# Kernel tuning notes

Measured on AMD Instinct MI355X. Metric: run time of the kernel, lower is better.

Reference implementation:

```python
import jax, jax.numpy as jnp
import numpy as np

B, T, D_IN, H, N_LAYERS, D_OUT = 256, 512, 128, 512, 3, 1


def setup_inputs() -> dict:
    key = jax.random.key(0)
    ks = jax.random.split(key, 20)
    s = 1.0 / np.sqrt(H)
    inp = {"x": jax.random.normal(ks[0], (B, T, D_IN), dtype=jnp.float32)}
    k = 1
    for l in range(N_LAYERS):
        d_in = D_IN if l == 0 else H
        inp[f"W_ih_{l}"] = jax.random.uniform(ks[k], (4 * H, d_in), minval=-s, maxval=s); k += 1
        inp[f"W_hh_{l}"] = jax.random.uniform(ks[k], (4 * H, H), minval=-s, maxval=s); k += 1
        inp[f"b_ih_{l}"] = jax.random.uniform(ks[k], (4 * H,), minval=-s, maxval=s); k += 1
        inp[f"b_hh_{l}"] = jax.random.uniform(ks[k], (4 * H,), minval=-s, maxval=s); k += 1
    inp["W_fc"] = jax.random.uniform(ks[k], (D_OUT, H), minval=-s, maxval=s); k += 1
    inp["b_fc"] = jax.random.uniform(ks[k], (D_OUT,), minval=-s, maxval=s)
    return inp


def _lstm_layer(x, W_ih, W_hh, b_ih, b_hh):
    # x: [B, T, d_in] -> hs: [B, T, H]. PyTorch gate order: i, f, g, o.
    xg = jnp.einsum("btd,gd->btg", x, W_ih) + b_ih + b_hh  # precompute input proj [B,T,4H]
    Hh = W_hh.shape[1]
    Bb = x.shape[0]

    def step(carry, xg_t):
        h, c = carry
        g = xg_t + h @ W_hh.T  # [B, 4H]
        i, f, gg, o = jnp.split(g, 4, axis=-1)
        c = jax.nn.sigmoid(f) * c + jax.nn.sigmoid(i) * jnp.tanh(gg)
        h = jax.nn.sigmoid(o) * jnp.tanh(c)
        return (h, c), h

    h0 = jnp.zeros((Bb, Hh), x.dtype)
    (_, _), hs = jax.lax.scan(step, (h0, h0), jnp.swapaxes(xg, 0, 1))
    return jnp.swapaxes(hs, 0, 1)


def reference(x, W_ih_0, W_hh_0, b_ih_0, b_hh_0,
              W_ih_1, W_hh_1, b_ih_1, b_hh_1,
              W_ih_2, W_hh_2, b_ih_2, b_hh_2,
              W_fc, b_fc):
    # Eval mode: inter-layer dropout (p=0.4) is identity.
    h = _lstm_layer(x, W_ih_0, W_hh_0, b_ih_0, b_hh_0)
    h = _lstm_layer(h, W_ih_1, W_hh_1, b_ih_1, b_hh_1)
    h = _lstm_layer(h, W_ih_2, W_hh_2, b_ih_2, b_hh_2)
    return h[:, -1, :] @ W_fc.T + b_fc  # [B, D_OUT]
```

## Files before the change

kernel.cpp:

```cpp
#include <hip/hip_runtime.h>

#define B_   256
#define T_   512
#define DIN_ 128
#define H_   512
#define G4_  2048

typedef __bf16 bf16_t;
typedef __bf16 bf16x8 __attribute__((ext_vector_type(8)));
typedef __bf16 bf16x4 __attribute__((ext_vector_type(4)));
typedef float  f32x4  __attribute__((ext_vector_type(4)));
typedef float  f32x16 __attribute__((ext_vector_type(16)));

__device__ __forceinline__ void gload16cc(const void* g, void* l) {
  __builtin_amdgcn_global_load_lds(
      (const __attribute__((address_space(1))) unsigned int*)g,
      (__attribute__((address_space(3))) unsigned int*)l, 16, 0, 17);
}
__device__ __forceinline__ int fload(const int* p) {
  return __hip_atomic_load(p, __ATOMIC_RELAXED, __HIP_MEMORY_SCOPE_AGENT);
}

__global__ void cast_f32_bf16(const float* __restrict__ s, bf16_t* __restrict__ d, int n) {
  int i = (blockIdx.x * 256 + threadIdx.x) * 4;
  if (i >= n) return;
  float4 v = *(const float4*)(s + i);
  bf16x4 o;
  o[0] = (bf16_t)v.x; o[1] = (bf16_t)v.y; o[2] = (bf16_t)v.z; o[3] = (bf16_t)v.w;
  *(bf16x4*)(d + i) = o;
}

__global__ void cast_strided(const float* __restrict__ s, bf16_t* __restrict__ d,
                             int Ks, int Kd, int coff) {
  int npr = Ks >> 3;
  int i = blockIdx.x * 256 + threadIdx.x;
  if (i >= 2048 * npr) return;
  int row = i / npr, j = i - row * npr;
  const float* sp = s + (size_t)row * Ks + j * 8;
  float4 v0 = *(const float4*)sp;
  float4 v1 = *(const float4*)(sp + 4);
  bf16x8 o;
  o[0] = (bf16_t)v0.x; o[1] = (bf16_t)v0.y; o[2] = (bf16_t)v0.z; o[3] = (bf16_t)v0.w;
  o[4] = (bf16_t)v1.x; o[5] = (bf16_t)v1.y; o[6] = (bf16_t)v1.z; o[7] = (bf16_t)v1.w;
  *(bf16x8*)(d + (size_t)row * Kd + coff + j * 8) = o;
}

__global__ void bias_sum(const float* __restrict__ a, const float* __restrict__ b,
                         float* __restrict__ o, int n) {
  int i = blockIdx.x * 256 + threadIdx.x;
  if (i < n) o[i] = a[i] + b[i];
}

#define RING_N (8 * 256 * 512)
#define XG_N   (8 * 256 * 2048)
#define FSTR   16

__device__ __forceinline__ void l0_loop(
    char* smem, const bf16_t* __restrict__ xbf, const bf16_t* __restrict__ wcl,
    const float* __restrict__ bias_l, bf16_t* ringOwn, int* flags, int* xgf,
    int bg, int ug)
{
  constexpr int ROWB = 1280;
  const int tid  = threadIdx.x;
  const int lane = tid & 63;
  const int wv   = tid >> 6;
  const int g    = wv & 3;
  const int kh   = wv >> 2;
  const int r32  = lane & 31;
  const int l5   = lane >> 5;
  const int u0   = ug * 32;
  const int t0x  = kh * 4;
  const int t0h  = 8 + kh * 16;

  bf16x8 wfrag[20];
  {
    const bf16_t* wrow = wcl + (size_t)(g * 512 + u0 + r32) * 640 + l5 * 8;
    #pragma unroll
    for (int i = 0; i < 4; ++i)  wfrag[i]     = *(const bf16x8*)(wrow + (t0x + i) * 16);
    #pragma unroll
    for (int i = 0; i < 16; ++i) wfrag[4 + i] = *(const bf16x8*)(wrow + (t0h + i) * 16);
  }
  const int um = tid >> 3;
  const int uq = tid & 7;
  float bsv[4][4];
  #pragma unroll
  for (int g2 = 0; g2 < 4; ++g2)
    #pragma unroll
    for (int q = 0; q < 4; ++q)
      bsv[g2][q] = bias_l[g2 * 512 + u0 + uq * 4 + q];

  float cst[4] = {0.f, 0.f, 0.f, 0.f};
  float* gp = (float*)smem;

  int* fl_own = flags + (0 * 4 + bg) * FSTR;
  int* bpf    = xgf + (0 * 4 + bg) * FSTR;

  for (int s = 0; s < 512; ++s) {
    const int slot  = s & 7;
    const int slot2 = (s - 1) & 7;
    {
      int r0 = tid >> 4, c0 = tid & 15;
      bf16x8 v0 = *(const bf16x8*)(xbf + ((size_t)(bg * 64 + r0) * T_ + s) * 128 + c0 * 8);
      int i1 = 512 + tid, r1 = i1 >> 4, c1 = i1 & 15;
      bf16x8 v1 = *(const bf16x8*)(xbf + ((size_t)(bg * 64 + r1) * T_ + s) * 128 + c1 * 8);
      *(bf16x8*)(smem + r0 * ROWB + (c0 ^ (r0 & 15)) * 16) = v0;
      *(bf16x8*)(smem + r1 * ROWB + (c1 ^ (r1 & 15)) * 16) = v1;
    }
    __syncthreads();
    f32x16 acc0 = {}, acc1 = {};
    #pragma unroll
    for (int i = 0; i < 2; ++i) {
      const int px = ((t0x + i) * 2 + l5) ^ (r32 & 15);
      bf16x8 a0 = *(const bf16x8*)(smem + r32 * ROWB + px * 16);
      bf16x8 a1 = *(const bf16x8*)(smem + (32 + r32) * ROWB + px * 16);
      acc0 = __builtin_amdgcn_mfma_f32_32x32x16_bf16(a0, wfrag[i], acc0, 0, 0, 0);
      acc1 = __builtin_amdgcn_mfma_f32_32x32x16_bf16(a1, wfrag[i], acc1, 0, 0, 0);
    }
    if (tid == 0) {
      if (s > 0)
        while (fload(fl_own + (s - 1) * 4 * FSTR) < 16) __builtin_amdgcn_s_sleep(1);
      if (s >= 8)
        while (fload(bpf + (s - 8) * 4 * FSTR) < 8) __builtin_amdgcn_s_sleep(1);
    }
    __syncthreads();
    {
      const bf16_t* ownS = ringOwn + (size_t)slot2 * (256 * 512) + (size_t)(bg * 64) * 512;
      #pragma unroll
      for (int i = 0; i < 8; ++i) {
        int r = i * 8 + wv;
        gload16cc(ownS + r * 512 + (lane ^ (r & 15)) * 8, smem + r * ROWB + 256);
      }
    }
    #pragma unroll
    for (int i = 2; i < 4; ++i) {
      const int px = ((t0x + i) * 2 + l5) ^ (r32 & 15);
      bf16x8 a0 = *(const bf16x8*)(smem + r32 * ROWB + px * 16);
      bf16x8 a1 = *(const bf16x8*)(smem + (32 + r32) * ROWB + px * 16);
      acc0 = __builtin_amdgcn_mfma_f32_32x32x16_bf16(a0, wfrag[i], acc0, 0, 0, 0);
      acc1 = __builtin_amdgcn_mfma_f32_32x32x16_bf16(a1, wfrag[i], acc1, 0, 0, 0);
    }
    __syncthreads();
    #pragma unroll
    for (int i = 0; i < 16; ++i) {
      const int px = ((t0h + i) * 2 + l5) ^ (r32 & 15);
      bf16x8 a0 = *(const bf16x8*)(smem + r32 * ROWB + px * 16);
      bf16x8 a1 = *(const bf16x8*)(smem + (32 + r32) * ROWB + px * 16);
      acc0 = __builtin_amdgcn_mfma_f32_32x32x16_bf16(a0, wfrag[4 + i], acc0, 0, 0, 0);
      acc1 = __builtin_amdgcn_mfma_f32_32x32x16_bf16(a1, wfrag[4 + i], acc1, 0, 0, 0);
    }
    __syncthreads();
    {
      const int base = kh * 8192 + g * 32 + r32;
      #pragma unroll
      for (int reg = 0; reg < 16; ++reg) {
        int mr = (reg & 3) + 8 * (reg >> 2) + 4 * l5;
        gp[base + mr * 128]        = acc0[reg];
        gp[base + (32 + mr) * 128] = acc1[reg];
      }
    }
    __syncthreads();
    union { bf16x4 v; unsigned long long u; } pk;
    {
      f32x4 gv[4];
      #pragma unroll
      for (int g2 = 0; g2 < 4; ++g2) {
        f32x4 p0 = *(const f32x4*)&gp[um * 128 + g2 * 32 + uq * 4];
        f32x4 p1 = *(const f32x4*)&gp[8192 + um * 128 + g2 * 32 + uq * 4];
        #pragma unroll
        for (int q = 0; q < 4; ++q) gv[g2][q] = p0[q] + p1[q];
      }
      #pragma unroll
      for (int q = 0; q < 4; ++q) {
        float i_ = gv[0][q] + bsv[0][q];
        float f_ = gv[1][q] + bsv[1][q];
        float g_ = gv[2][q] + bsv[2][q];
        float o_ = gv[3][q] + bsv[3][q];
        float si = 1.f / (1.f + __expf(-i_));
        float sf = 1.f / (1.f + __expf(-f_));
        float so = 1.f / (1.f + __expf(-o_));
        float tg = 2.f / (1.f + __expf(-2.f * g_)) - 1.f;
        float cv = sf * cst[q] + si * tg;
        cst[q] = cv;
        float th = 2.f / (1.f + __expf(-2.f * cv)) - 1.f;
        pk.v[q] = (bf16_t)(so * th);
      }
    }
    {
      int b = bg * 64 + um;
      bf16_t* dst = ringOwn + (size_t)slot * (256 * 512) + (size_t)b * 512 + u0 + uq * 4;
      (void)__hip_atomic_exchange((unsigned long long*)dst, pk.u,
                                  __ATOMIC_RELAXED, __HIP_MEMORY_SCOPE_AGENT);
    }
    __syncthreads();
    if (tid == 0) atomicAdd(fl_own + s * 4 * FSTR, 1);
  }
}

__device__ __forceinline__ void main_loop(
    char* smem, const bf16_t* __restrict__ wcl, const float* __restrict__ bias_l,
    const float* __restrict__ xgRing, bf16_t* ringOwn, float* __restrict__ hsf,
    int* flags, int* xgf, int layer, int bg, int ug)
{
  const int tid  = threadIdx.x;
  const int lane = tid & 63;
  const int wv   = tid >> 6;
  const int g    = wv & 3;
  const int kh   = wv >> 2;
  const int r32  = lane & 31;
  const int l5   = lane >> 5;
  const int u0   = ug * 32;

  bf16x8 wfrag[16];
  {
    const bf16_t* wrow = wcl + (size_t)(g * 512 + u0 + r32) * 1024 + 512 + kh * 256 + l5 * 8;
    #pragma unroll
    for (int i = 0; i < 16; ++i) wfrag[i] = *(const bf16x8*)(wrow + i * 16);
  }
  const int um = tid >> 3;
  const int uq = tid & 7;
  float bsv[4][4];
  #pragma unroll
  for (int g2 = 0; g2 < 4; ++g2)
    #pragma unroll
    for (int q = 0; q < 4; ++q)
      bsv[g2][q] = bias_l[g2 * 512 + u0 + uq * 4 + q];

  float cst[4] = {0.f, 0.f, 0.f, 0.f};

  int* fl_own = flags + ((layer * 512) * 4 + bg) * FSTR;
  int* xgf_in = xgf + (((layer - 1) * 512) * 4 + bg) * FSTR;
  int* xgf_bp = xgf + ((1 * 512) * 4 + bg) * FSTR;

  for (int s = 0; s < 512; ++s) {
    const int slot  = s & 7;
    const int slot2 = (s - 1) & 7;
    if (tid == 0) {
      while (fload(xgf_in + s * 4 * FSTR) < 8) __builtin_amdgcn_s_sleep(1);
      if (s > 0)
        while (fload(fl_own + (s - 1) * 4 * FSTR) < 16) __builtin_amdgcn_s_sleep(1);
      if (layer == 1 && s >= 8)
        while (fload(xgf_bp + (s - 8) * 4 * FSTR) < 8) __builtin_amdgcn_s_sleep(1);
    }
    __syncthreads();
    {
      const bf16_t* ownS = ringOwn + (size_t)slot2 * (256 * 512) + (size_t)(bg * 64) * 512;
      #pragma unroll
      for (int i = 0; i < 8; ++i) {
        int r = i * 8 + wv;
        gload16cc(ownS + r * 512 + (lane ^ (r & 15)) * 8, smem + r * 1024);
      }
      const float* xgS = xgRing + (size_t)slot * (256 * 2048) + (size_t)(bg * 64) * 2048;
      #pragma unroll
      for (int i = 0; i < 4; ++i) {
        int id = (i * 8 + wv) * 64 + lane;
        int row = id >> 5, sub = id & 31, g2 = sub >> 3, cp = sub & 7;
        gload16cc(xgS + (size_t)row * 2048 + g2 * 512 + u0 + cp * 4,
                  smem + 65536 + (i * 8 + wv) * 1024);
      }
    }
    __syncthreads();
    f32x16 acc0 = {}, acc1 = {};
    #pragma unroll
    for (int i = 0; i < 16; ++i) {
      const int c  = (kh * 16 + i) * 2 + l5;
      const int px = c ^ (r32 & 15);
      bf16x8 a0 = *(const bf16x8*)(smem + r32 * 1024 + px * 16);
      bf16x8 a1 = *(const bf16x8*)(smem + (32 + r32) * 1024 + px * 16);
      acc0 = __builtin_amdgcn_mfma_f32_32x32x16_bf16(a0, wfrag[i], acc0, 0, 0, 0);
      acc1 = __builtin_amdgcn_mfma_f32_32x32x16_bf16(a1, wfrag[i], acc1, 0, 0, 0);
    }
    __syncthreads();
    {
      char* pb = smem + kh * 32768 + (g * 32 + r32) * 4;
      #pragma unroll
      for (int reg = 0; reg < 16; ++reg) {
        int mr = (reg & 3) + 8 * (reg >> 2) + 4 * l5;
        *(float*)(pb + mr * 512)        = acc0[reg];
        *(float*)(pb + (32 + mr) * 512) = acc1[reg];
      }
    }
    __syncthreads();
    union { bf16x4 v; unsigned long long u; } pk;
    f32x4 hvf;
    {
      const char* gpb = smem + um * 512;
      const char* xgb = smem + 65536 + um * 512;
      f32x4 gvv[4];
      #pragma unroll
      for (int g2 = 0; g2 < 4; ++g2) {
        f32x4 p0 = *(const f32x4*)(gpb + (g2 * 32 + uq * 4) * 4);
        f32x4 p1 = *(const f32x4*)(gpb + 32768 + (g2 * 32 + uq * 4) * 4);
        f32x4 xv = *(const f32x4*)(xgb + g2 * 128 + uq * 16);
        #pragma unroll
        for (int q = 0; q < 4; ++q) gvv[g2][q] = p0[q] + p1[q] + xv[q];
      }
      #pragma unroll
      for (int q = 0; q < 4; ++q) {
        float i_ = gvv[0][q] + bsv[0][q];
        float f_ = gvv[1][q] + bsv[1][q];
        float g_ = gvv[2][q] + bsv[2][q];
        float o_ = gvv[3][q] + bsv[3][q];
        float si = 1.f / (1.f + __expf(-i_));
        float sf = 1.f / (1.f + __expf(-f_));
        float so = 1.f / (1.f + __expf(-o_));
        float tg = 2.f / (1.f + __expf(-2.f * g_)) - 1.f;
        float cv = sf * cst[q] + si * tg;
        cst[q] = cv;
        float th = 2.f / (1.f + __expf(-2.f * cv)) - 1.f;
        hvf[q] = so * th;
        pk.v[q] = (bf16_t)hvf[q];
      }
    }
    {
      int b = bg * 64 + um;
      bf16_t* dst = ringOwn + (size_t)slot * (256 * 512) + (size_t)b * 512 + u0 + uq * 4;
      (void)__hip_atomic_exchange((unsigned long long*)dst, pk.u,
                                  __ATOMIC_RELAXED, __HIP_MEMORY_SCOPE_AGENT);
      if (layer == 2 && s == 511)
        *(f32x4*)(hsf + (size_t)b * 512 + u0 + uq * 4) = hvf;
    }
    __syncthreads();
    if (tid == 0) atomicAdd(fl_own + s * 4 * FSTR, 1);
  }
}

__device__ __forceinline__ void helper_loop(
    char* smem, const bf16_t* __restrict__ wihl, const bf16_t* __restrict__ ringPrev,
    float* __restrict__ xgRing, int* flags, int* xgf, int hl, int bg, int ng)
{
  const int tid  = threadIdx.x;
  const int lane = tid & 63;
  const int wv   = tid >> 6;
  const int r32  = lane & 31;
  const int l5   = lane >> 5;
  const int n0   = ng * 256 + wv * 32;

  bf16x8 wfrag[32];
  {
    const bf16_t* wrow = wihl + (size_t)(n0 + r32) * 1024 + l5 * 8;
    #pragma unroll
    for (int i = 0; i < 32; ++i) wfrag[i] = *(const bf16x8*)(wrow + i * 16);
  }
  int* fl_prev = flags + (((hl - 1) * 512) * 4 + bg) * FSTR;
  int* fl_cons = flags + ((hl * 512) * 4 + bg) * FSTR;
  int* xgf_own = xgf + (((hl - 1) * 512) * 4 + bg) * FSTR;

  for (int s = 0; s < 512; ++s) {
    const int slot = s & 7;
    if (tid == 0) {
      while (fload(fl_prev + s * 4 * FSTR) < 16) __builtin_amdgcn_s_sleep(1);
      if (s >= 8)
        while (fload(fl_cons + (s - 8) * 4 * FSTR) < 16) __builtin_amdgcn_s_sleep(1);
    }
    __syncthreads();
    {
      const bf16_t* src = ringPrev + (size_t)slot * (256 * 512) + (size_t)(bg * 64) * 512;
      #pragma unroll
      for (int i = 0; i < 8; ++i) {
        int r = i * 8 + wv;
        gload16cc(src + r * 512 + (lane ^ (r & 15)) * 8, smem + r * 1024);
      }
    }
    __syncthreads();
    f32x16 acc0 = {}, acc1 = {};
    #pragma unroll
    for (int i = 0; i < 32; ++i) {
      const int px = (i * 2 + l5) ^ (r32 & 15);
      bf16x8 a0 = *(const bf16x8*)(smem + r32 * 1024 + px * 16);
      bf16x8 a1 = *(const bf16x8*)(smem + (32 + r32) * 1024 + px * 16);
      acc0 = __builtin_amdgcn_mfma_f32_32x32x16_bf16(a0, wfrag[i], acc0, 0, 0, 0);
      acc1 = __builtin_amdgcn_mfma_f32_32x32x16_bf16(a1, wfrag[i], acc1, 0, 0, 0);
    }
    {
      float* dst = xgRing + (size_t)slot * (256 * 2048) + (size_t)(bg * 64) * 2048 + n0 + r32;
      #pragma unroll
      for (int reg = 0; reg < 16; ++reg) {
        int mr = (reg & 3) + 8 * (reg >> 2) + 4 * l5;
        __hip_atomic_store(dst + (size_t)mr * 2048, acc0[reg],
                           __ATOMIC_RELAXED, __HIP_MEMORY_SCOPE_AGENT);
        __hip_atomic_store(dst + (size_t)(32 + mr) * 2048, acc1[reg],
                           __ATOMIC_RELAXED, __HIP_MEMORY_SCOPE_AGENT);
      }
    }
    __syncthreads();
    if (tid == 0) atomicAdd(xgf_own + s * 4 * FSTR, 1);
  }
}

__global__ __launch_bounds__(512, 2)
void lstm_persist(const bf16_t* __restrict__ xbf, const bf16_t* __restrict__ wc,
                  const float* __restrict__ bias, bf16_t* __restrict__ rings,
                  float* __restrict__ xg, float* __restrict__ hsf,
                  int* __restrict__ flags)
{
  __shared__ __align__(16) char smem[131072];
  int* xgf = flags + 3 * 512 * 4 * FSTR;
  const int bid = blockIdx.x;
  if (bid < 192) {
    const int layer = bid >> 6;
    const int bg    = (bid >> 4) & 3;
    const int ug    = bid & 15;
    bf16_t* ringOwn = rings + (size_t)layer * RING_N;
    if (layer == 0) {
      l0_loop(smem, xbf, wc, bias, ringOwn, flags, xgf, bg, ug);
    } else {
      const bf16_t* wcl = wc + 2048 * 640 + (size_t)(layer - 1) * 2048 * 1024;
      const float* xgR  = xg + (size_t)(layer - 1) * XG_N;
      main_loop(smem, wcl, bias + layer * 2048, xgR, ringOwn, hsf, flags, xgf,
                layer, bg, ug);
    }
  } else {
    const int hid = bid - 192;
    const int hl  = 1 + (hid >> 5);
    const int bg  = (hid >> 3) & 3;
    const int ng  = hid & 7;
    const bf16_t* wihl = wc + 2048 * 640 + (size_t)(hl - 1) * 2048 * 1024;
    const bf16_t* ringPrev = rings + (size_t)(hl - 1) * RING_N;
    float* xgR = xg + (size_t)(hl - 1) * XG_N;
    helper_loop(smem, wihl, ringPrev, xgR, flags, xgf, hl, bg, ng);
  }
}

__global__ void fc_kernel(const float* __restrict__ h, const float* __restrict__ Wfc,
                          const float* __restrict__ bfc, float* __restrict__ out) {
  int b = blockIdx.x;
  int l = threadIdx.x;
  const float* hp = h + (size_t)b * H_;
  float acc = 0.f;
  #pragma unroll
  for (int i = 0; i < 8; ++i) acc += hp[l + i * 64] * Wfc[l + i * 64];
  #pragma unroll
  for (int off = 32; off; off >>= 1) acc += __shfl_down(acc, off, 64);
  if (l == 0) out[b] = acc + bfc[0];
}

extern "C" void kernel_launch(void* const* d_in, const int* in_sizes, int n_in,
                              void* d_out, int out_size, void* d_ws, size_t ws_size,
                              hipStream_t stream) {
  const float* x        = (const float*)d_in[0];
  const float* Wih_f[3] = {(const float*)d_in[1], (const float*)d_in[5], (const float*)d_in[9]};
  const float* Whh_f[3] = {(const float*)d_in[2], (const float*)d_in[6], (const float*)d_in[10]};
  const float* bih_f[3] = {(const float*)d_in[3], (const float*)d_in[7], (const float*)d_in[11]};
  const float* bhh_f[3] = {(const float*)d_in[4], (const float*)d_in[8], (const float*)d_in[12]};
  const float* Wfc = (const float*)d_in[13];
  const float* bfc = (const float*)d_in[14];

  const size_t FLAGS_BYTES = (size_t)(3 * 512 * 4 + 2 * 512 * 4) * FSTR * 4;

  char* ws = (char*)d_ws;
  size_t off = 0;
  auto take = [&](size_t bytes) { char* p = ws + off; off = (off + bytes + 255) & ~255ULL; return p; };
  bf16_t* XBF   = (bf16_t*)take((size_t)B_ * T_ * DIN_ * 2);
  bf16_t* WC    = (bf16_t*)take((size_t)(2048*640 + 2*2048*1024) * 2);
  float*  BIAS  = (float*) take(3 * 2048 * 4);
  bf16_t* RINGS = (bf16_t*)take((size_t)3 * RING_N * 2);
  float*  XG    = (float*) take((size_t)2 * XG_N * 4);
  float*  HSF   = (float*) take((size_t)B_ * H_ * 4);
  int*    FLAGS = (int*)   take(FLAGS_BYTES);

  bf16_t* WC1 = WC + 2048 * 640;
  bf16_t* WC2 = WC1 + 2048 * 1024;

  cast_f32_bf16<<<16384, 256, 0, stream>>>(x, XBF, B_ * T_ * DIN_);
  cast_strided<<<128, 256, 0, stream>>>(Wih_f[0], WC,  128, 640, 0);
  cast_strided<<<512, 256, 0, stream>>>(Whh_f[0], WC,  512, 640, 128);
  cast_strided<<<512, 256, 0, stream>>>(Wih_f[1], WC1, 512, 1024, 0);
  cast_strided<<<512, 256, 0, stream>>>(Whh_f[1], WC1, 512, 1024, 512);
  cast_strided<<<512, 256, 0, stream>>>(Wih_f[2], WC2, 512, 1024, 0);
  cast_strided<<<512, 256, 0, stream>>>(Whh_f[2], WC2, 512, 1024, 512);
  for (int l = 0; l < 3; ++l)
    bias_sum<<<8, 256, 0, stream>>>(bih_f[l], bhh_f[l], BIAS + l * 2048, G4_);
  hipMemsetAsync(RINGS, 0, (size_t)3 * RING_N * 2, stream);
  hipMemsetAsync(FLAGS, 0, FLAGS_BYTES, stream);

  lstm_persist<<<256, 512, 0, stream>>>(XBF, WC, BIAS, RINGS, XG, HSF, FLAGS);
  fc_kernel<<<B_, 64, 0, stream>>>(HSF, Wfc, bfc, (float*)d_out);
}
```

Baseline: 3.311 ms.

## Offload layer-0 input projection to helper blocks via a 16-slot xg ring

Layer-0 recurrent blocks previously computed the x·W_ih projection inline on every step, which lengthens the serial critical path. Helper blocks now compute that projection 8 steps ahead, using their spare upper waves, and write it into a new 16-slot fp32 ring guarded by a new flag array. Layer 0 then runs the same templated main_loop as the other layers and only reads the precomputed gates. The cost is extra helper work, fp32 ring traffic and extra flag synchronisation.

```diff
diff --git a/kernel.cpp b/kernel.cpp
--- a/kernel.cpp
+++ b/kernel.cpp
@@ -51,16 +51,21 @@
   if (i < n) o[i] = a[i] + b[i];
 }
 
-#define RING_N (8 * 256 * 512)
-#define XG_N   (8 * 256 * 2048)
-#define FSTR   16
-
-__device__ __forceinline__ void l0_loop(
-    char* smem, const bf16_t* __restrict__ xbf, const bf16_t* __restrict__ wcl,
-    const float* __restrict__ bias_l, bf16_t* ringOwn, int* flags, int* xgf,
-    int bg, int ug)
+#define RING_N  (8 * 256 * 512)
+#define XG_N    (8 * 256 * 2048)
+#define XG0_N   (16 * 256 * 2048)
+#define FSTR    16
+
+template<int LAYER>
+__device__ __forceinline__ void main_loop(
+    char* smem, const bf16_t* __restrict__ wcl, const float* __restrict__ bias_l,
+    const float* __restrict__ xgRing, bf16_t* ringOwn, float* __restrict__ hsf,
+    int* flags, int* xgf, int* xgf0, int bg, int ug)
 {
-  constexpr int ROWB = 1280;
+  constexpr int KLW   = LAYER ? 1024 : 640;
+  constexpr int WOFF  = LAYER ? 512 : 128;
+  constexpr int XMASK = LAYER ? 7 : 15;
+  constexpr int XTH   = LAYER ? 8 : 16;
   const int tid  = threadIdx.x;
   const int lane = tid & 63;
   const int wv   = tid >> 6;
@@ -69,16 +74,12 @@
   const int r32  = lane & 31;
   const int l5   = lane >> 5;
   const int u0   = ug * 32;
-  const int t0x  = kh * 4;
-  const int t0h  = 8 + kh * 16;
-
-  bf16x8 wfrag[20];
+
+  bf16x8 wfrag[16];
   {
-    const bf16_t* wrow = wcl + (size_t)(g * 512 + u0 + r32) * 640 + l5 * 8;
+    const bf16_t* wrow = wcl + (size_t)(g * 512 + u0 + r32) * KLW + WOFF + kh * 256 + l5 * 8;
     #pragma unroll
-    for (int i = 0; i < 4; ++i)  wfrag[i]     = *(const bf16x8*)(wrow + (t0x + i) * 16);
-    #pragma unroll
-    for (int i = 0; i < 16; ++i) wfrag[4 + i] = *(const bf16x8*)(wrow + (t0h + i) * 16);
+    for (int i = 0; i < 16; ++i) wfrag[i] = *(const bf16x8*)(wrow + i * 16);
   }
   const int um = tid >> 3;
   const int uq = tid & 7;
@@ -90,156 +91,24 @@
       bsv[g2][q] = bias_l[g2 * 512 + u0 + uq * 4 + q];
 
   float cst[4] = {0.f, 0.f, 0.f, 0.f};
-  float* gp = (float*)smem;
-
-  int* fl_own = flags + (0 * 4 + bg) * FSTR;
-  int* bpf    = xgf + (0 * 4 + bg) * FSTR;
+
+  int* fl_own = flags + ((LAYER * 512) * 4 + bg) * FSTR;
+  int* xin    = (LAYER == 0) ? (xgf0 + bg * FSTR)
+                             : (xgf + (((LAYER - 1) * 512) * 4 + bg) * FSTR);
+  int* bp     = (LAYER == 0) ? (xgf + (0 * 4 + bg) * FSTR)
+              : (LAYER == 1) ? (xgf + ((1 * 512) * 4 + bg) * FSTR)
+              : (int*)nullptr;
 
   for (int s = 0; s < 512; ++s) {
     const int slot  = s & 7;
     const int slot2 = (s - 1) & 7;
-    {
-      int r0 = tid >> 4, c0 = tid & 15;
-      bf16x8 v0 = *(const bf16x8*)(xbf + ((size_t)(bg * 64 + r0) * T_ + s) * 128 + c0 * 8);
-      int i1 = 512 + tid, r1 = i1 >> 4, c1 = i1 & 15;
-      bf16x8 v1 = *(const bf16x8*)(xbf + ((size_t)(bg * 64 + r1) * T_ + s) * 128 + c1 * 8);
-      *(bf16x8*)(smem + r0 * ROWB + (c0 ^ (r0 & 15)) * 16) = v0;
-      *(bf16x8*)(smem + r1 * ROWB + (c1 ^ (r1 & 15)) * 16) = v1;
-    }
-    __syncthreads();
-    f32x16 acc0 = {}, acc1 = {};
-    #pragma unroll
-    for (int i = 0; i < 2; ++i) {
-      const int px = ((t0x + i) * 2 + l5) ^ (r32 & 15);
-      bf16x8 a0 = *(const bf16x8*)(smem + r32 * ROWB + px * 16);
-      bf16x8 a1 = *(const bf16x8*)(smem + (32 + r32) * ROWB + px * 16);
-      acc0 = __builtin_amdgcn_mfma_f32_32x32x16_bf16(a0, wfrag[i], acc0, 0, 0, 0);
-      acc1 = __builtin_amdgcn_mfma_f32_32x32x16_bf16(a1, wfrag[i], acc1, 0, 0, 0);
-    }
+    const int xslot = s & XMASK;
     if (tid == 0) {
+      while (fload(xin + s * 4 * FSTR) < XTH) __builtin_amdgcn_s_sleep(1);
       if (s > 0)
         while (fload(fl_own + (s - 1) * 4 * FSTR) < 16) __builtin_amdgcn_s_sleep(1);
-      if (s >= 8)
-        while (fload(bpf + (s - 8) * 4 * FSTR) < 8) __builtin_amdgcn_s_sleep(1);
-    }
-    __syncthreads();
-    {
-      const bf16_t* ownS = ringOwn + (size_t)slot2 * (256 * 512) + (size_t)(bg * 64) * 512;
-      #pragma unroll
-      for (int i = 0; i < 8; ++i) {
-        int r = i * 8 + wv;
-        gload16cc(ownS + r * 512 + (lane ^ (r & 15)) * 8, smem + r * ROWB + 256);
-      }
-    }
-    #pragma unroll
-    for (int i = 2; i < 4; ++i) {
-      const int px = ((t0x + i) * 2 + l5) ^ (r32 & 15);
-      bf16x8 a0 = *(const bf16x8*)(smem + r32 * ROWB + px * 16);
-      bf16x8 a1 = *(const bf16x8*)(smem + (32 + r32) * ROWB + px * 16);
-      acc0 = __builtin_amdgcn_mfma_f32_32x32x16_bf16(a0, wfrag[i], acc0, 0, 0, 0);
-      acc1 = __builtin_amdgcn_mfma_f32_32x32x16_bf16(a1, wfrag[i], acc1, 0, 0, 0);
-    }
-    __syncthreads();
-    #pragma unroll
-    for (int i = 0; i < 16; ++i) {
-      const int px = ((t0h + i) * 2 + l5) ^ (r32 & 15);
-      bf16x8 a0 = *(const bf16x8*)(smem + r32 * ROWB + px * 16);
-      bf16x8 a1 = *(const bf16x8*)(smem + (32 + r32) * ROWB + px * 16);
-      acc0 = __builtin_amdgcn_mfma_f32_32x32x16_bf16(a0, wfrag[4 + i], acc0, 0, 0, 0);
-      acc1 = __builtin_amdgcn_mfma_f32_32x32x16_bf16(a1, wfrag[4 + i], acc1, 0, 0, 0);
-    }
-    __syncthreads();
-    {
-      const int base = kh * 8192 + g * 32 + r32;
-      #pragma unroll
-      for (int reg = 0; reg < 16; ++reg) {
-        int mr = (reg & 3) + 8 * (reg >> 2) + 4 * l5;
-        gp[base + mr * 128]        = acc0[reg];
-        gp[base + (32 + mr) * 128] = acc1[reg];
-      }
-    }
-    __syncthreads();
-    union { bf16x4 v; unsigned long long u; } pk;
-    {
-      f32x4 gv[4];
-      #pragma unroll
-      for (int g2 = 0; g2 < 4; ++g2) {
-        f32x4 p0 = *(const f32x4*)&gp[um * 128 + g2 * 32 + uq * 4];
-        f32x4 p1 = *(const f32x4*)&gp[8192 + um * 128 + g2 * 32 + uq * 4];
-        #pragma unroll
-        for (int q = 0; q < 4; ++q) gv[g2][q] = p0[q] + p1[q];
-      }
-      #pragma unroll
-      for (int q = 0; q < 4; ++q) {
-        float i_ = gv[0][q] + bsv[0][q];
-        float f_ = gv[1][q] + bsv[1][q];
-        float g_ = gv[2][q] + bsv[2][q];
-        float o_ = gv[3][q] + bsv[3][q];
-        float si = 1.f / (1.f + __expf(-i_));
-        float sf = 1.f / (1.f + __expf(-f_));
-        float so = 1.f / (1.f + __expf(-o_));
-        float tg = 2.f / (1.f + __expf(-2.f * g_)) - 1.f;
-        float cv = sf * cst[q] + si * tg;
-        cst[q] = cv;
-        float th = 2.f / (1.f + __expf(-2.f * cv)) - 1.f;
-        pk.v[q] = (bf16_t)(so * th);
-      }
-    }
-    {
-      int b = bg * 64 + um;
-      bf16_t* dst = ringOwn + (size_t)slot * (256 * 512) + (size_t)b * 512 + u0 + uq * 4;
-      (void)__hip_atomic_exchange((unsigned long long*)dst, pk.u,
-                                  __ATOMIC_RELAXED, __HIP_MEMORY_SCOPE_AGENT);
-    }
-    __syncthreads();
-    if (tid == 0) atomicAdd(fl_own + s * 4 * FSTR, 1);
-  }
-}
-
-__device__ __forceinline__ void main_loop(
-    char* smem, const bf16_t* __restrict__ wcl, const float* __restrict__ bias_l,
-    const float* __restrict__ xgRing, bf16_t* ringOwn, float* __restrict__ hsf,
-    int* flags, int* xgf, int layer, int bg, int ug)
-{
-  const int tid  = threadIdx.x;
-  const int lane = tid & 63;
-  const int wv   = tid >> 6;
-  const int g    = wv & 3;
-  const int kh   = wv >> 2;
-  const int r32  = lane & 31;
-  const int l5   = lane >> 5;
-  const int u0   = ug * 32;
-
-  bf16x8 wfrag[16];
-  {
-    const bf16_t* wrow = wcl + (size_t)(g * 512 + u0 + r32) * 1024 + 512 + kh * 256 + l5 * 8;
-    #pragma unroll
-    for (int i = 0; i < 16; ++i) wfrag[i] = *(const bf16x8*)(wrow + i * 16);
-  }
-  const int um = tid >> 3;
-  const int uq = tid & 7;
-  float bsv[4][4];
-  #pragma unroll
-  for (int g2 = 0; g2 < 4; ++g2)
-    #pragma unroll
-    for (int q = 0; q < 4; ++q)
-      bsv[g2][q] = bias_l[g2 * 512 + u0 + uq * 4 + q];
-
-  float cst[4] = {0.f, 0.f, 0.f, 0.f};
-
-  int* fl_own = flags + ((layer * 512) * 4 + bg) * FSTR;
-  int* xgf_in = xgf + (((layer - 1) * 512) * 4 + bg) * FSTR;
-  int* xgf_bp = xgf + ((1 * 512) * 4 + bg) * FSTR;
-
-  for (int s = 0; s < 512; ++s) {
-    const int slot  = s & 7;
-    const int slot2 = (s - 1) & 7;
-    if (tid == 0) {
-      while (fload(xgf_in + s * 4 * FSTR) < 8) __builtin_amdgcn_s_sleep(1);
-      if (s > 0)
-        while (fload(fl_own + (s - 1) * 4 * FSTR) < 16) __builtin_amdgcn_s_sleep(1);
-      if (layer == 1 && s >= 8)
-        while (fload(xgf_bp + (s - 8) * 4 * FSTR) < 8) __builtin_amdgcn_s_sleep(1);
+      if (LAYER < 2 && s >= 8)
+        while (fload(bp + (s - 8) * 4 * FSTR) < 8) __builtin_amdgcn_s_sleep(1);
     }
     __syncthreads();
     {
@@ -249,7 +118,7 @@
         int r = i * 8 + wv;
         gload16cc(ownS + r * 512 + (lane ^ (r & 15)) * 8, smem + r * 1024);
       }
-      const float* xgS = xgRing + (size_t)slot * (256 * 2048) + (size_t)(bg * 64) * 2048;
+      const float* xgS = xgRing + (size_t)xslot * (256 * 2048) + (size_t)(bg * 64) * 2048;
       #pragma unroll
       for (int i = 0; i < 4; ++i) {
         int id = (i * 8 + wv) * 64 + lane;
@@ -316,7 +185,7 @@
       bf16_t* dst = ringOwn + (size_t)slot * (256 * 512) + (size_t)b * 512 + u0 + uq * 4;
       (void)__hip_atomic_exchange((unsigned long long*)dst, pk.u,
                                   __ATOMIC_RELAXED, __HIP_MEMORY_SCOPE_AGENT);
-      if (layer == 2 && s == 511)
+      if (LAYER == 2 && s == 511)
         *(f32x4*)(hsf + (size_t)b * 512 + u0 + uq * 4) = hvf;
     }
     __syncthreads();
@@ -324,9 +193,12 @@
   }
 }
 
+template<int HL>
 __device__ __forceinline__ void helper_loop(
-    char* smem, const bf16_t* __restrict__ wihl, const bf16_t* __restrict__ ringPrev,
-    float* __restrict__ xgRing, int* flags, int* xgf, int hl, int bg, int ng)
+    char* smem, const bf16_t* __restrict__ wihl, const bf16_t* __restrict__ wc0,
+    const bf16_t* __restrict__ xbf, const bf16_t* __restrict__ ringPrev,
+    float* __restrict__ xgRing, float* __restrict__ xg0Ring,
+    int* flags, int* xgf, int* xgf0, int bg, int ng)
 {
   const int tid  = threadIdx.x;
   const int lane = tid & 63;
@@ -334,6 +206,7 @@
   const int r32  = lane & 31;
   const int l5   = lane >> 5;
   const int n0   = ng * 256 + wv * 32;
+  const int cs   = (HL - 1) * 8 + ng;
 
   bf16x8 wfrag[32];
   {
@@ -341,19 +214,22 @@
     #pragma unroll
     for (int i = 0; i < 32; ++i) wfrag[i] = *(const bf16x8*)(wrow + i * 16);
   }
-  int* fl_prev = flags + (((hl - 1) * 512) * 4 + bg) * FSTR;
-  int* fl_cons = flags + ((hl * 512) * 4 + bg) * FSTR;
-  int* xgf_own = xgf + (((hl - 1) * 512) * 4 + bg) * FSTR;
-
-  for (int s = 0; s < 512; ++s) {
-    const int slot = s & 7;
-    if (tid == 0) {
+  int* fl_prev  = flags + (((HL - 1) * 512) * 4 + bg) * FSTR;
+  int* fl_cons  = flags + ((HL * 512) * 4 + bg) * FSTR;
+  int* xgf_own  = xgf + (((HL - 1) * 512) * 4 + bg) * FSTR;
+  int* xgf0_own = xgf0 + bg * FSTR;
+
+  for (int s = -8; s < 512; ++s) {
+    const bool doH = (s >= 0);
+    const bool doX = (s + 8 < 512);
+    const int  slot = s & 7;
+    if (doH && tid == 0) {
       while (fload(fl_prev + s * 4 * FSTR) < 16) __builtin_amdgcn_s_sleep(1);
       if (s >= 8)
         while (fload(fl_cons + (s - 8) * 4 * FSTR) < 16) __builtin_amdgcn_s_sleep(1);
     }
     __syncthreads();
-    {
+    if (doH) {
       const bf16_t* src = ringPrev + (size_t)slot * (256 * 512) + (size_t)(bg * 64) * 512;
       #pragma unroll
       for (int i = 0; i < 8; ++i) {
@@ -361,17 +237,25 @@
         gload16cc(src + r * 512 + (lane ^ (r & 15)) * 8, smem + r * 1024);
       }
     }
-    __syncthreads();
-    f32x16 acc0 = {}, acc1 = {};
-    #pragma unroll
-    for (int i = 0; i < 32; ++i) {
-      const int px = (i * 2 + l5) ^ (r32 & 15);
-      bf16x8 a0 = *(const bf16x8*)(smem + r32 * 1024 + px * 16);
-      bf16x8 a1 = *(const bf16x8*)(smem + (32 + r32) * 1024 + px * 16);
-      acc0 = __builtin_amdgcn_mfma_f32_32x32x16_bf16(a0, wfrag[i], acc0, 0, 0, 0);
-      acc1 = __builtin_amdgcn_mfma_f32_32x32x16_bf16(a1, wfrag[i], acc1, 0, 0, 0);
-    }
-    {
+    if (doX) {
+      #pragma unroll
+      for (int i2 = 0; i2 < 2; ++i2) {
+        int id = i2 * 512 + tid, r = id >> 4, cx = id & 15;
+        bf16x8 v = *(const bf16x8*)(xbf + ((size_t)(bg * 64 + r) * T_ + (s + 8)) * 128 + cx * 8);
+        *(bf16x8*)(smem + 65536 + r * 256 + (cx ^ (r & 15)) * 16) = v;
+      }
+    }
+    __syncthreads();
+    if (doH) {
+      f32x16 acc0 = {}, acc1 = {};
+      #pragma unroll
+      for (int i = 0; i < 32; ++i) {
+        const int px = (i * 2 + l5) ^ (r32 & 15);
+        bf16x8 a0 = *(const bf16x8*)(smem + r32 * 1024 + px * 16);
+        bf16x8 a1 = *(const bf16x8*)(smem + (32 + r32) * 1024 + px * 16);
+        acc0 = __builtin_amdgcn_mfma_f32_32x32x16_bf16(a0, wfrag[i], acc0, 0, 0, 0);
+        acc1 = __builtin_amdgcn_mfma_f32_32x32x16_bf16(a1, wfrag[i], acc1, 0, 0, 0);
+      }
       float* dst = xgRing + (size_t)slot * (256 * 2048) + (size_t)(bg * 64) * 2048 + n0 + r32;
       #pragma unroll
       for (int reg = 0; reg < 16; ++reg) {
@@ -382,42 +266,74 @@
                            __ATOMIC_RELAXED, __HIP_MEMORY_SCOPE_AGENT);
       }
     }
-    __syncthreads();
-    if (tid == 0) atomicAdd(xgf_own + s * 4 * FSTR, 1);
+    if (doX && wv >= 4) {
+      bf16x8 wf0[8];
+      const bf16_t* w0 = wc0 + (size_t)(cs * 128 + (wv - 4) * 32 + r32) * 640 + l5 * 8;
+      #pragma unroll
+      for (int t = 0; t < 8; ++t) wf0[t] = *(const bf16x8*)(w0 + t * 16);
+      f32x16 x0 = {}, x1 = {};
+      #pragma unroll
+      for (int t = 0; t < 8; ++t) {
+        const int px = (t * 2 + l5) ^ (r32 & 15);
+        bf16x8 a0 = *(const bf16x8*)(smem + 65536 + r32 * 256 + px * 16);
+        bf16x8 a1 = *(const bf16x8*)(smem + 65536 + (32 + r32) * 256 + px * 16);
+        x0 = __builtin_amdgcn_mfma_f32_32x32x16_bf16(a0, wf0[t], x0, 0, 0, 0);
+        x1 = __builtin_amdgcn_mfma_f32_32x32x16_bf16(a1, wf0[t], x1, 0, 0, 0);
+      }
+      float* dst0 = xg0Ring + (size_t)((s + 8) & 15) * (256 * 2048)
+                  + (size_t)(bg * 64) * 2048 + cs * 128 + (wv - 4) * 32 + r32;
+      #pragma unroll
+      for (int reg = 0; reg < 16; ++reg) {
+        int mr = (reg & 3) + 8 * (reg >> 2) + 4 * l5;
+        __hip_atomic_store(dst0 + (size_t)mr * 2048, x0[reg],
+                           __ATOMIC_RELAXED, __HIP_MEMORY_SCOPE_AGENT);
+        __hip_atomic_store(dst0 + (size_t)(32 + mr) * 2048, x1[reg],
+                           __ATOMIC_RELAXED, __HIP_MEMORY_SCOPE_AGENT);
+      }
+    }
+    __syncthreads();
+    if (tid == 0) {
+      if (doH) atomicAdd(xgf_own + s * 4 * FSTR, 1);
+      if (doX) atomicAdd(xgf0_own + (s + 8) * 4 * FSTR, 1);
+    }
   }
 }
 
 __global__ __launch_bounds__(512, 2)
 void lstm_persist(const bf16_t* __restrict__ xbf, const bf16_t* __restrict__ wc,
                   const float* __restrict__ bias, bf16_t* __restrict__ rings,
-                  float* __restrict__ xg, float* __restrict__ hsf,
-                  int* __restrict__ flags)
+                  float* __restrict__ xg, float* __restrict__ xg0,
+                  float* __restrict__ hsf, int* __restrict__ flags)
 {
   __shared__ __align__(16) char smem[131072];
-  int* xgf = flags + 3 * 512 * 4 * FSTR;
+  int* xgf  = flags + 3 * 512 * 4 * FSTR;
+  int* xgf0 = xgf + 2 * 512 * 4 * FSTR;
   const int bid = blockIdx.x;
+  const bf16_t* wc1 = wc + 2048 * 640;
+  const bf16_t* wc2 = wc1 + 2048 * 1024;
   if (bid < 192) {
     const int layer = bid >> 6;
     const int bg    = (bid >> 4) & 3;
     const int ug    = bid & 15;
     bf16_t* ringOwn = rings + (size_t)layer * RING_N;
-    if (layer == 0) {
-      l0_loop(smem, xbf, wc, bias, ringOwn, flags, xgf, bg, ug);
-    } else {
-      const bf16_t* wcl = wc + 2048 * 640 + (size_t)(layer - 1) * 2048 * 1024;
-      const float* xgR  = xg + (size_t)(layer - 1) * XG_N;
-      main_loop(smem, wcl, bias + layer * 2048, xgR, ringOwn, hsf, flags, xgf,
-                layer, bg, ug);
-    }
+    if (layer == 0)
+      main_loop<0>(smem, wc,  bias,        xg0,        ringOwn, hsf, flags, xgf, xgf0, bg, ug);
+    else if (layer == 1)
+      main_loop<1>(smem, wc1, bias + 2048, xg,         ringOwn, hsf, flags, xgf, xgf0, bg, ug);
+    else
+      main_loop<2>(smem, wc2, bias + 4096, xg + XG_N,  ringOwn, hsf, flags, xgf, xgf0, bg, ug);
   } else {
     const int hid = bid - 192;
     const int hl  = 1 + (hid >> 5);
     const int bg  = (hid >> 3) & 3;
     const int ng  = hid & 7;
-    const bf16_t* wihl = wc + 2048 * 640 + (size_t)(hl - 1) * 2048 * 1024;
+    const bf16_t* wihl = (hl == 1) ? wc1 : wc2;
     const bf16_t* ringPrev = rings + (size_t)(hl - 1) * RING_N;
     float* xgR = xg + (size_t)(hl - 1) * XG_N;
-    helper_loop(smem, wihl, ringPrev, xgR, flags, xgf, hl, bg, ng);
+    if (hl == 1)
+      helper_loop<1>(smem, wihl, wc, xbf, ringPrev, xgR, xg0, flags, xgf, xgf0, bg, ng);
+    else
+      helper_loop<2>(smem, wihl, wc, xbf, ringPrev, xgR, xg0, flags, xgf, xgf0, bg, ng);
   }
 }
 
@@ -445,7 +361,7 @@
   const float* Wfc = (const float*)d_in[13];
   const float* bfc = (const float*)d_in[14];
 
-  const size_t FLAGS_BYTES = (size_t)(3 * 512 * 4 + 2 * 512 * 4) * FSTR * 4;
+  const size_t FLAGS_BYTES = (size_t)(3 * 512 * 4 + 2 * 512 * 4 + 512 * 4) * FSTR * 4;
 
   char* ws = (char*)d_ws;
   size_t off = 0;
@@ -455,6 +371,7 @@
   float*  BIAS  = (float*) take(3 * 2048 * 4);
   bf16_t* RINGS = (bf16_t*)take((size_t)3 * RING_N * 2);
   float*  XG    = (float*) take((size_t)2 * XG_N * 4);
+  float*  XG0   = (float*) take((size_t)XG0_N * 4);
   float*  HSF   = (float*) take((size_t)B_ * H_ * 4);
   int*    FLAGS = (int*)   take(FLAGS_BYTES);
 
@@ -473,6 +390,6 @@
   hipMemsetAsync(RINGS, 0, (size_t)3 * RING_N * 2, stream);
   hipMemsetAsync(FLAGS, 0, FLAGS_BYTES, stream);
 
-  lstm_persist<<<256, 512, 0, stream>>>(XBF, WC, BIAS, RINGS, XG, HSF, FLAGS);
+  lstm_persist<<<256, 512, 0, stream>>>(XBF, WC, BIAS, RINGS, XG, XG0, HSF, FLAGS);
   fc_kernel<<<B_, 64, 0, stream>>>(HSF, Wfc, bfc, (float*)d_out);
 }
```

Result: slower. 5.006 ms (+51.2%).
